# Kernel optimization log

Measured on AMD Instinct MI355X. Metric: run time of the kernel, lower is better.

The kernel has to match this reference:

```python
import jax, jax.numpy as jnp
import numpy as np

# ---- module hyperparameters ----
B, L, F = 128, 720, 128
SEG = 24            # segment_length
NSEG = L // SEG     # 30 input segments
WIN = 15            # window_size
NPRED = 96 // SEG   # 4 prediction segments
D = 128             # encode_dim
H = 512             # hidden_dim
DECAY = 0.9
C = 1.0             # curvature
EPS = 1e-6
MAXN = 1.0 - 1e-5   # max radius of Poincare ball (c=1)
SQC = 1.0           # sqrt(C)

# ---- Poincare-ball manifold ops ----
def _sqnorm(x):
    return jnp.sum(x * x, axis=-1, keepdims=True)

def _norm(x):
    return jnp.sqrt(jnp.maximum(_sqnorm(x), EPS * EPS))

def _project(x):
    n = _norm(x)
    return jnp.where(n > MAXN, x * (MAXN / n), x)

def _artanh(x):
    return jnp.arctanh(jnp.clip(x, -1.0 + 1e-7, 1.0 - 1e-7))

def mobius_add(x, y):
    xy = jnp.sum(x * y, axis=-1, keepdims=True)
    x2, y2 = _sqnorm(x), _sqnorm(y)
    num = (1.0 + 2.0 * C * xy + C * y2) * x + (1.0 - C * x2) * y
    den = 1.0 + 2.0 * C * xy + C * C * x2 * y2
    return num / jnp.maximum(den, EPS)

def expmap0(v):
    n = _norm(v)
    return _project(jnp.tanh(SQC * n) * v / (SQC * n))

def logmap0(y):
    n = _norm(y)
    return _artanh(SQC * n) * y / (SQC * n)

def expmap(x, v):
    lam = 2.0 / jnp.maximum(1.0 - C * _sqnorm(x), EPS)
    n = _norm(v)
    second = jnp.tanh(SQC * lam * n / 2.0) * v / (SQC * n)
    return _project(mobius_add(x, second))

def logmap(x, y):
    d = mobius_add(-x, y)
    n = _norm(d)
    lam = 2.0 / jnp.maximum(1.0 - C * _sqnorm(x), EPS)
    return (2.0 / (SQC * lam)) * _artanh(SQC * n) * d / n


def setup_inputs() -> dict:
    key = jax.random.key(0)
    ks = jax.random.split(key, 12)
    s = 0.05
    return {
        'trend':           0.5 * jax.random.normal(ks[0], (B, L, F), jnp.float32),
        'seasonal_coarse': 0.5 * jax.random.normal(ks[1], (B, L, F), jnp.float32),
        'seasonal_fine':   0.5 * jax.random.normal(ks[2], (B, L, F), jnp.float32),
        'residual':        0.5 * jax.random.normal(ks[3], (B, L, F), jnp.float32),
        'W_t': s * jax.random.normal(ks[4], (SEG, D), jnp.float32), 'b_t': jnp.zeros((D,), jnp.float32),
        'W_c': s * jax.random.normal(ks[5], (SEG, D), jnp.float32), 'b_c': jnp.zeros((D,), jnp.float32),
        'W_f': s * jax.random.normal(ks[6], (SEG, D), jnp.float32), 'b_f': jnp.zeros((D,), jnp.float32),
        'W_r': s * jax.random.normal(ks[7], (SEG, D), jnp.float32), 'b_r': jnp.zeros((D,), jnp.float32),
        'alpha': jnp.array([0.5], jnp.float32),
        'W1': s * jax.random.normal(ks[8], (D, H), jnp.float32), 'b1': jnp.zeros((H,), jnp.float32),
        'W2': s * jax.random.normal(ks[9], (H, SEG), jnp.float32), 'b2': jnp.zeros((SEG,), jnp.float32),
    }


def reference(trend, seasonal_coarse, seasonal_fine, residual,
              W_t, b_t, W_c, b_c, W_f, b_f, W_r, b_r,
              alpha, W1, b1, W2, b2):
    b, l, f = trend.shape

    def collapse(x):  # [B,L,F] -> [B*F, NSEG, SEG]
        return x.transpose(0, 2, 1).reshape(b * f, NSEG, SEG)

    t_s, c_s, f_s, r_s = map(collapse, (trend, seasonal_coarse, seasonal_fine, residual))

    # per-segment tangent encoding (channel-independent, shared params)
    tan = (jnp.einsum('bns,sd->bnd', t_s, W_t) + b_t
           + jnp.einsum('bns,sd->bnd', c_s, W_c) + b_c
           + jnp.einsum('bns,sd->bnd', f_s, W_f) + b_f
           + jnp.einsum('bns,sd->bnd', r_s, W_r) + b_r)
    z = expmap0(tan)                     # [BF, NSEG, D] on the ball
    z_cur = z[:, -WIN:, :]

    idx = jnp.arange(WIN - 1, dtype=jnp.float32)
    w = DECAY ** (WIN - 2 - idx)
    w = w / w.sum()

    preds, latents = [], []
    for _ in range(NPRED):
        z_last = z_cur[:, -1]
        vel = logmap(z_cur[:, :-1], z_cur[:, 1:])
        avg_v = jnp.sum(vel * w[None, :, None], axis=1)    # [BF, D]
        z_next = expmap(z_last, alpha * avg_v)             # dynamics step
        latents.append(z_next)
        # reconstruction head: logmap0 -> MLP -> segment
        t0 = logmap0(z_next)
        seg = jax.nn.relu(t0 @ W1 + b1) @ W2 + b2          # [BF, SEG]
        preds.append(seg)
        z_cur = jnp.concatenate([z_cur[:, 1:], z_next[:, None]], axis=1)

    p = jnp.stack(preds, axis=1).reshape(b * f, NPRED * SEG)
    predictions = p.reshape(b, f, NPRED * SEG).transpose(0, 2, 1)  # [B, pred_len, F]
    return predictions
```

## Files before the change

### kernel.cpp

```cpp
#include <hip/hip_runtime.h>
#include <hip/hip_bf16.h>

namespace {
constexpr int kL = 720, kF = 128;
constexpr int kWin = 15;
constexpr float kEps = 1e-6f;
constexpr float kMaxN = 1.0f - 1e-5f;
constexpr int kT0off = 360;
constexpr int XROW = 388;
constexpr int ZTR = 132;
constexpr size_t kOffT0   = 0;
constexpr size_t kOffW1   = 16777216;
constexpr size_t kOffW2   = kOffW1 + 131072;
constexpr size_t kOffWcat = kOffW2 + 32768;
constexpr size_t kOffBsum = kOffWcat + 49152;
constexpr size_t kOffHid  = 17825792;
constexpr size_t kWsSplit = kOffHid + 67108864;
}

typedef float f32x4 __attribute__((ext_vector_type(4)));
typedef short s16x8 __attribute__((ext_vector_type(8)));

__device__ __forceinline__ float rcp_f(float x) { return __builtin_amdgcn_rcpf(x); }
__device__ __forceinline__ float sqrt_f(float x) { return __builtin_amdgcn_sqrtf(x); }
__device__ __forceinline__ float tanh_f(float x) {
  float t = __builtin_amdgcn_exp2f(x * -2.8853900817779268f);
  return (1.0f - t) * rcp_f(1.0f + t);
}
__device__ __forceinline__ float artanh_f(float n) {
  float nc = fminf(n, 1.0f - 1e-7f);
  return 0.34657359027997264f * __builtin_amdgcn_logf((1.0f + nc) * rcp_f(1.0f - nc));
}

extern "C" __global__ __launch_bounds__(256)
void mwhf_prep(const float* __restrict__ W1, const float* __restrict__ W2,
               const float* __restrict__ W_t, const float* __restrict__ W_c,
               const float* __restrict__ W_f, const float* __restrict__ W_r,
               const float* __restrict__ b_t, const float* __restrict__ b_c,
               const float* __restrict__ b_f, const float* __restrict__ b_r,
               __hip_bfloat16* __restrict__ W1bf, __hip_bfloat16* __restrict__ W2bf,
               float* __restrict__ Wcat, float* __restrict__ bsum)
{
  const int b = blockIdx.x, tid = threadIdx.x;
  if (b < 64) {
    const int n0 = b * 8;
    for (int e = tid; e < 1024; e += 256) {
      int n_l = e & 7, k = e >> 3;
      W1bf[(size_t)(n0 + n_l) * 128 + k] = __float2bfloat16(W1[(size_t)k * 512 + n0 + n_l]);
    }
  } else if (b < 68) {
    const int k0 = (b - 64) * 128;
    for (int e = tid; e < 4096; e += 256) {
      int p = e >> 7, k_l = e & 127;
      float v = (p < 24) ? W2[(size_t)(k0 + k_l) * 24 + p] : 0.0f;
      W2bf[(size_t)p * 512 + k0 + k_l] = __float2bfloat16(v);
    }
  } else if (b < 72) {
    const int st = b - 68;
    const float* src = (st == 0) ? W_t : (st == 1) ? W_c : (st == 2) ? W_f : W_r;
    for (int e = tid; e < 3072; e += 256) Wcat[st * 3072 + e] = src[e];
  } else {
    if (tid < 128) bsum[tid] = b_t[tid] + b_c[tid] + b_f[tid] + b_r[tid];
  }
}

extern "C" __global__ __launch_bounds__(256, 4)
void mwhf_k1(const float* __restrict__ trend,
             const float* __restrict__ seas_c,
             const float* __restrict__ seas_f,
             const float* __restrict__ resid,
             const float* __restrict__ Wcat, const float* __restrict__ bsum,
             const float* __restrict__ alpha,
             __hip_bfloat16* __restrict__ t0_out)
{
  __shared__ float ublk[4 * kWin * ZTR];
  __shared__ float z2t[64];

  const int tid = threadIdx.x;
  const int bix = blockIdx.x;
  const int bb = (bix & 7) * 16 + (bix >> 8);
  const int f0 = ((bix >> 3) & 31) * 4;
  const int row0 = bb * 128 + f0;

  {
    float* xs = ublk;
    const float* ptrs[4] = {trend, seas_c, seas_f, resid};
    for (int e = tid; e < 1440; e += 256) {
      int seg = e / 96;
      int k = e - seg * 96;
      int st = k / 24, s = k - st * 24;
      const float* p = ptrs[st];
      float4 v = *(const float4*)&p[(size_t)(bb * kL + kT0off + seg * 24 + s) * kF + f0];
      *(float4*)&ublk[seg * XROW + k * 4] = v;
      (void)xs;
    }
  }
  __syncthreads();

  const int seg = tid >> 4;
  const int dg  = tid & 15;
  const bool act = (seg < kWin);
  float acc[4][8];
  float scale4[4], zz24[4];
  if (act) {
#pragma unroll
    for (int r = 0; r < 4; ++r)
#pragma unroll
      for (int j = 0; j < 8; ++j) acc[r][j] = 0.f;
    const float* xrow = &ublk[seg * XROW];
    const float* wp = Wcat + dg * 8;
#pragma unroll 4
    for (int k = 0; k < 96; ++k) {
      float4 x4 = *(const float4*)&xrow[k * 4];
      float4 wa = *(const float4*)&wp[k * 128];
      float4 wb = *(const float4*)&wp[k * 128 + 4];
      float w8[8] = {wa.x, wa.y, wa.z, wa.w, wb.x, wb.y, wb.z, wb.w};
#pragma unroll
      for (int j = 0; j < 8; ++j) {
        acc[0][j] += x4.x * w8[j];
        acc[1][j] += x4.y * w8[j];
        acc[2][j] += x4.z * w8[j];
        acc[3][j] += x4.w * w8[j];
      }
    }
    float b8[8];
    *(float4*)&b8[0] = *(const float4*)&bsum[dg * 8];
    *(float4*)&b8[4] = *(const float4*)&bsum[dg * 8 + 4];
    float part[4];
#pragma unroll
    for (int r = 0; r < 4; ++r) {
      part[r] = 0.f;
#pragma unroll
      for (int j = 0; j < 8; ++j) {
        acc[r][j] += b8[j];
        part[r] += acc[r][j] * acc[r][j];
      }
    }
#pragma unroll
    for (int m = 1; m <= 8; m <<= 1)
#pragma unroll
      for (int r = 0; r < 4; ++r) part[r] += __shfl_xor(part[r], m);
#pragma unroll
    for (int r = 0; r < 4; ++r) {
      float v2 = part[r];
      float nv = sqrt_f(fmaxf(v2, 1e-12f));
      float sc = tanh_f(nv) * rcp_f(nv);
      float y2 = sc * sc * v2;
      float yn = sqrt_f(fmaxf(y2, 1e-12f));
      float proj = (yn > kMaxN) ? (kMaxN * rcp_f(yn)) : 1.0f;
      scale4[r] = sc * proj;
      zz24[r] = y2 * proj * proj;
    }
  }
  __syncthreads();
  if (act) {
#pragma unroll
    for (int r = 0; r < 4; ++r) {
      float o8[8];
#pragma unroll
      for (int j = 0; j < 8; ++j) o8[j] = acc[r][j] * scale4[r];
      float* zp = &ublk[(r * kWin + seg) * ZTR + dg * 8];
      *(float4*)&zp[0] = *(const float4*)&o8[0];
      *(float4*)&zp[4] = *(const float4*)&o8[4];
      if (dg == 0) z2t[r * 16 + seg] = zz24[r];
    }
  }
  __syncthreads();

  {
    const int w = tid >> 6;
    const int l = tid & 63;
    float zx[19], zy[19], z2a[19], pd[18];
#pragma unroll
    for (int j = 0; j < 15; ++j) {
      float2 v = *(const float2*)&ublk[(w * kWin + j) * ZTR + 2 * l];
      zx[j] = v.x; zy[j] = v.y;
      z2a[j] = z2t[w * 16 + j];
    }
#pragma unroll
    for (int j = 0; j < 14; ++j) pd[j] = zx[j] * zx[j + 1] + zy[j] * zy[j + 1];
#pragma unroll
    for (int m = 1; m <= 32; m <<= 1)
#pragma unroll
      for (int j = 0; j < 14; ++j) pd[j] += __shfl_xor(pd[j], m);

    const float alp = alpha[0];
    float W14[14];
    {
      float wv = 1.f, ss = 0.f;
      W14[13] = 1.f;
#pragma unroll
      for (int i = 12; i >= 0; --i) { wv *= 0.9f; W14[i] = wv; }
#pragma unroll
      for (int i = 0; i < 14; ++i) ss += W14[i];
      float inv = 1.f / ss;
#pragma unroll
      for (int i = 0; i < 14; ++i) W14[i] *= inv;
    }

#pragma unroll
    for (int it = 0; it < 4; ++it) {
      float avx = 0.f, avy = 0.f;
#pragma unroll
      for (int i = 0; i < 14; ++i) {
        const int j = it + i, y = j + 1;
        float x2 = z2a[j], y2 = z2a[y], dp = pd[j];
        float A = 1.f - 2.f * dp + y2;
        float Bq = 1.f - x2;
        float den = fmaxf(1.f - 2.f * dp + x2 * y2, kEps);
        float invd = rcp_f(den);
        float d2 = (A * A * x2 - 2.f * A * Bq * dp + Bq * Bq * y2) * (invd * invd);
        float n = sqrt_f(fmaxf(d2, 1e-12f));
        float coef = fmaxf(Bq, kEps) * artanh_f(n) * rcp_f(n);
        float wi = W14[i] * coef * invd;
        avx += wi * (Bq * zx[y] - A * zx[j]);
        avy += wi * (Bq * zy[y] - A * zy[j]);
      }
      float vx = alp * avx, vy = alp * avy;
      const int pl = it + 14;
      float x2l = z2a[pl];
      float v2 = vx * vx + vy * vy;
      float xdv = zx[pl] * vx + zy[pl] * vy;
#pragma unroll
      for (int m = 1; m <= 32; m <<= 1) {
        v2 += __shfl_xor(v2, m);
        xdv += __shfl_xor(xdv, m);
      }
      float nv = sqrt_f(fmaxf(v2, 1e-12f));
      float lam = 2.f * rcp_f(fmaxf(1.f - x2l, kEps));
      float co = tanh_f(0.5f * lam * nv) * rcp_f(nv);
      float s2 = co * co * v2;
      float xy = co * xdv;
      float P = 1.f + 2.f * xy + s2;
      float Q = 1.f - x2l;
      float den2 = fmaxf(1.f + 2.f * xy + x2l * s2, kEps);
      float invd2 = rcp_f(den2);
      float znx = (P * zx[pl] + Q * co * vx) * invd2;
      float zny = (P * zy[pl] + Q * co * vy) * invd2;
      float zn2 = (P * P * x2l + 2.f * P * Q * xy + Q * Q * s2) * (invd2 * invd2);
      float pdn = (P * x2l + Q * xy) * invd2;
      float yn = sqrt_f(fmaxf(zn2, 1e-12f));
      float proj = (yn > kMaxN) ? (kMaxN * rcp_f(yn)) : 1.f;
      znx *= proj; zny *= proj;
      zn2 *= proj * proj;
      pdn *= proj;
      zx[15 + it] = znx; zy[15 + it] = zny;
      z2a[15 + it] = zn2;
      pd[14 + it] = pdn;
      float n0 = sqrt_f(fmaxf(zn2, 1e-12f));
      float fac = artanh_f(n0) * rcp_f(n0);
      __hip_bfloat162 hv;
      hv.x = __float2bfloat16(fac * znx);
      hv.y = __float2bfloat16(fac * zny);
      *(__hip_bfloat162*)(t0_out + ((size_t)(row0 + w) * 4 + it) * 128 + 2 * l) = hv;
    }
  }
}

extern "C" __global__ __launch_bounds__(256, 4)
void mwhf_k2a(const __hip_bfloat16* __restrict__ t0g,
              const __hip_bfloat16* __restrict__ W1bf,
              const float* __restrict__ b1,
              __hip_bfloat16* __restrict__ hid)
{
  const int tid = threadIdx.x;
  const int w = tid >> 6, lane = tid & 63;
  const int l16 = lane & 15, quad = lane >> 4;
  const int mbase = blockIdx.x * 32;
  const int ng = w * 128;

  s16x8 afr[2][4];
#pragma unroll
  for (int s = 0; s < 2; ++s)
#pragma unroll
    for (int kc = 0; kc < 4; ++kc)
      afr[s][kc] = *(const s16x8*)(t0g + (size_t)(mbase + s * 16 + l16) * 128 + kc * 32 + quad * 8);

  f32x4 acc[2][8];
#pragma unroll
  for (int s = 0; s < 2; ++s)
#pragma unroll
    for (int t = 0; t < 8; ++t) acc[s][t] = (f32x4)0.f;

#pragma unroll
  for (int t = 0; t < 8; ++t) {
    const __hip_bfloat16* bp = W1bf + (size_t)(ng + t * 16 + l16) * 128 + quad * 8;
#pragma unroll
    for (int kc = 0; kc < 4; ++kc) {
      s16x8 bfr = *(const s16x8*)(bp + kc * 32);
      acc[0][t] = __builtin_amdgcn_mfma_f32_16x16x32_bf16(afr[0][kc], bfr, acc[0][t], 0, 0, 0);
      acc[1][t] = __builtin_amdgcn_mfma_f32_16x16x32_bf16(afr[1][kc], bfr, acc[1][t], 0, 0, 0);
    }
  }
#pragma unroll
  for (int t = 0; t < 8; ++t) {
    const int n = ng + t * 16 + l16;
    float bv = b1[n];
#pragma unroll
    for (int s = 0; s < 2; ++s)
#pragma unroll
      for (int r = 0; r < 4; ++r) {
        int m = mbase + s * 16 + quad * 4 + r;
        float h = fmaxf(acc[s][t][r] + bv, 0.f);
        hid[(size_t)m * 512 + n] = __float2bfloat16(h);
      }
  }
}

extern "C" __global__ __launch_bounds__(256, 4)
void mwhf_k2b(const __hip_bfloat16* __restrict__ hid,
              const __hip_bfloat16* __restrict__ W2bf,
              const float* __restrict__ b2,
              float* __restrict__ outp)
{
  const int tid = threadIdx.x;
  const int w = tid >> 6, lane = tid & 63;
  const int l16 = lane & 15, quad = lane >> 4;
  const int mb = (blockIdx.x * 4 + w) * 32;

  f32x4 acc[2][2];
#pragma unroll
  for (int s = 0; s < 2; ++s)
#pragma unroll
    for (int t = 0; t < 2; ++t) acc[s][t] = (f32x4)0.f;

#pragma unroll 4
  for (int kc = 0; kc < 16; ++kc) {
    s16x8 a0 = *(const s16x8*)(hid + (size_t)(mb + l16) * 512 + kc * 32 + quad * 8);
    s16x8 a1 = *(const s16x8*)(hid + (size_t)(mb + 16 + l16) * 512 + kc * 32 + quad * 8);
#pragma unroll
    for (int t = 0; t < 2; ++t) {
      s16x8 bfr = *(const s16x8*)(W2bf + (size_t)(t * 16 + l16) * 512 + kc * 32 + quad * 8);
      acc[0][t] = __builtin_amdgcn_mfma_f32_16x16x32_bf16(a0, bfr, acc[0][t], 0, 0, 0);
      acc[1][t] = __builtin_amdgcn_mfma_f32_16x16x32_bf16(a1, bfr, acc[1][t], 0, 0, 0);
    }
  }
#pragma unroll
  for (int t = 0; t < 2; ++t) {
    const int p = t * 16 + l16;
    if (p < 24) {
      float bv = b2[p];
#pragma unroll
      for (int s = 0; s < 2; ++s)
#pragma unroll
        for (int r = 0; r < 4; ++r) {
          int m = mb + s * 16 + quad * 4 + r;
          int bbi = m >> 9, it = m & 3, f = (m >> 2) & 127;
          outp[(size_t)bbi * 12288 + (it * 24 + p) * 128 + f] = acc[s][t][r] + bv;
        }
    }
  }
}

extern "C" __global__ __launch_bounds__(256)
void mwhf_k2f(const __hip_bfloat16* __restrict__ t0g,
              const __hip_bfloat16* __restrict__ W1bf,
              const __hip_bfloat16* __restrict__ W2bf,
              const float* __restrict__ b1, const float* __restrict__ b2,
              float* __restrict__ outp)
{
  __shared__ __align__(16) char smem[147456];
  s16x8* Av   = (s16x8*)smem;
  s16x8* W1v  = (s16x8*)(smem + 16384);
  s16x8* W2v  = (s16x8*)(smem + 16384);
  float* red  = (float*)(smem + 49152);
  __hip_bfloat16* hid = (__hip_bfloat16*)(smem + 81920);
  s16x8* hidv = (s16x8*)(smem + 81920);

  const int tid = threadIdx.x;
  const int m0 = blockIdx.x * 64;
  const int w = tid >> 6, lane = tid & 63;
  const int l16 = lane & 15, quad = lane >> 4;

  {
    const s16x8* src = (const s16x8*)(t0g + (size_t)m0 * 128);
    for (int e = tid; e < 1024; e += 256) {
      int m = e >> 4, c = e & 15;
      Av[m * 16 + (c ^ (m & 7))] = src[e];
    }
  }
  f32x4 acc[4][4];
  for (int nh = 0; nh < 2; ++nh) {
    __syncthreads();
    {
      const s16x8* src = (const s16x8*)W1bf + (size_t)nh * 4096;
      for (int e = tid; e < 4096; e += 256) {
        int n = e >> 4, c = e & 15;
        W1v[n * 16 + (c ^ (n & 7))] = src[e];
      }
    }
    __syncthreads();
#pragma unroll
    for (int s = 0; s < 4; ++s)
#pragma unroll
      for (int t = 0; t < 4; ++t) acc[s][t] = (f32x4)0.f;
#pragma unroll
    for (int ks = 0; ks < 4; ++ks) {
      s16x8 a[4];
#pragma unroll
      for (int s = 0; s < 4; ++s)
        a[s] = Av[(s * 16 + l16) * 16 + ((ks * 4 + quad) ^ (l16 & 7))];
#pragma unroll
      for (int t = 0; t < 4; ++t) {
        int nl = w * 64 + t * 16 + l16;
        s16x8 bfr = W1v[nl * 16 + ((ks * 4 + quad) ^ (nl & 7))];
#pragma unroll
        for (int s = 0; s < 4; ++s)
          acc[s][t] = __builtin_amdgcn_mfma_f32_16x16x32_bf16(a[s], bfr, acc[s][t], 0, 0, 0);
      }
    }
#pragma unroll
    for (int t = 0; t < 4; ++t) {
      int nabs = nh * 256 + w * 64 + t * 16 + l16;
      float bv = b1[nabs];
#pragma unroll
      for (int s = 0; s < 4; ++s)
#pragma unroll
        for (int r = 0; r < 4; ++r) {
          int m = s * 16 + quad * 4 + r;
          float h = fmaxf(acc[s][t][r] + bv, 0.f);
          hid[m * 512 + (nabs ^ ((m & 7) << 3))] = __float2bfloat16(h);
        }
    }
  }
  __syncthreads();
  {
    const s16x8* src = (const s16x8*)W2bf;
    for (int e = tid; e < 2048; e += 256) {
      int p = e >> 6, c = e & 63;
      W2v[p * 64 + (c ^ (p & 7))] = src[e];
    }
  }
  __syncthreads();
  {
    f32x4 a2[2];
    a2[0] = (f32x4)0.f; a2[1] = (f32x4)0.f;
    const int m = w * 16 + l16;
#pragma unroll 4
    for (int ks = 0; ks < 16; ++ks) {
      s16x8 av = hidv[m * 64 + ((ks * 4 + quad) ^ (l16 & 7))];
#pragma unroll
      for (int t = 0; t < 2; ++t) {
        s16x8 bfr = W2v[(t * 16 + l16) * 64 + ((ks * 4 + quad) ^ (l16 & 7))];
        a2[t] = __builtin_amdgcn_mfma_f32_16x16x32_bf16(av, bfr, a2[t], 0, 0, 0);
      }
    }
#pragma unroll
    for (int t = 0; t < 2; ++t)
#pragma unroll
      for (int r = 0; r < 4; ++r) {
        int p = t * 16 + l16;
        if (p < 24) red[(w * 16 + quad * 4 + r) * 25 + p] = a2[t][r];
      }
  }
  __syncthreads();
  {
    const int bbi = m0 >> 9;
    const int f0 = (m0 >> 2) & 127;
    for (int e = tid; e < 1536; e += 256) {
      int fi = e & 15;
      int rest = e >> 4;
      int p = rest % 24;
      int it = rest / 24;
      outp[(size_t)bbi * 12288 + rest * 128 + f0 + fi] = red[(fi * 4 + it) * 25 + p] + b2[p];
    }
  }
}

extern "C" void kernel_launch(void* const* d_in, const int* in_sizes, int n_in,
                              void* d_out, int out_size, void* d_ws, size_t ws_size,
                              hipStream_t stream) {
  (void)in_sizes; (void)n_in; (void)out_size;
  const float* trend = (const float*)d_in[0];
  const float* sc    = (const float*)d_in[1];
  const float* sf    = (const float*)d_in[2];
  const float* rs    = (const float*)d_in[3];
  const float* W_t   = (const float*)d_in[4];
  const float* b_t   = (const float*)d_in[5];
  const float* W_c   = (const float*)d_in[6];
  const float* b_c   = (const float*)d_in[7];
  const float* W_f   = (const float*)d_in[8];
  const float* b_f   = (const float*)d_in[9];
  const float* W_r   = (const float*)d_in[10];
  const float* b_r   = (const float*)d_in[11];
  const float* alpha = (const float*)d_in[12];
  const float* W1    = (const float*)d_in[13];
  const float* b1    = (const float*)d_in[14];
  const float* W2    = (const float*)d_in[15];
  const float* b2    = (const float*)d_in[16];

  char* ws = (char*)d_ws;
  __hip_bfloat16* t0   = (__hip_bfloat16*)(ws + kOffT0);
  __hip_bfloat16* W1bf = (__hip_bfloat16*)(ws + kOffW1);
  __hip_bfloat16* W2bf = (__hip_bfloat16*)(ws + kOffW2);
  float* Wcat = (float*)(ws + kOffWcat);
  float* bsum = (float*)(ws + kOffBsum);
  __hip_bfloat16* hid = (__hip_bfloat16*)(ws + kOffHid);
  float* outp = (float*)d_out;

  hipLaunchKernelGGL(mwhf_prep, dim3(73), dim3(256), 0, stream,
                     W1, W2, W_t, W_c, W_f, W_r, b_t, b_c, b_f, b_r,
                     W1bf, W2bf, Wcat, bsum);
  hipLaunchKernelGGL(mwhf_k1, dim3(4096), dim3(256), 0, stream,
                     trend, sc, sf, rs, Wcat, bsum, alpha, t0);
  if (ws_size >= kWsSplit) {
    hipLaunchKernelGGL(mwhf_k2a, dim3(2048), dim3(256), 0, stream, t0, W1bf, b1, hid);
    hipLaunchKernelGGL(mwhf_k2b, dim3(512), dim3(256), 0, stream, hid, W2bf, b2, outp);
  } else {
    hipLaunchKernelGGL(mwhf_k2f, dim3(1024), dim3(256), 0, stream,
                       t0, W1bf, W2bf, b1, b2, outp);
  }
}
```

Before: 390.1 us.

## Compute segment encoder GEMM with split-bf16 MFMA instead of scalar FP32

Replaces the scalar FP32 FMA loop for the segment-encoding projection with bf16 MFMA instructions. Both inputs and weights are split into three bf16 pieces (hi/mid/lo) so that near-FP32 accuracy is kept using six MFMAs per tile. The weights are pre-split and transposed in the prep kernel, and the input tile is split on load into LDS. The occupancy hint is lowered from 4 to 3 blocks, and the extra split/convert work adds VALU and LDS traffic in exchange for the MFMA throughput.

```diff
diff --git a/kernel.cpp b/kernel.cpp
--- a/kernel.cpp
+++ b/kernel.cpp
@@ -7,13 +7,13 @@
 constexpr float kEps = 1e-6f;
 constexpr float kMaxN = 1.0f - 1e-5f;
 constexpr int kT0off = 360;
-constexpr int XROW = 388;
 constexpr int ZTR = 132;
+constexpr int AROW = 104;
 constexpr size_t kOffT0   = 0;
 constexpr size_t kOffW1   = 16777216;
 constexpr size_t kOffW2   = kOffW1 + 131072;
-constexpr size_t kOffWcat = kOffW2 + 32768;
-constexpr size_t kOffBsum = kOffWcat + 49152;
+constexpr size_t kOffBt   = kOffW2 + 32768;
+constexpr size_t kOffBsum = kOffBt + 73728;
 constexpr size_t kOffHid  = 17825792;
 constexpr size_t kWsSplit = kOffHid + 67108864;
 }
@@ -39,7 +39,8 @@
                const float* __restrict__ b_t, const float* __restrict__ b_c,
                const float* __restrict__ b_f, const float* __restrict__ b_r,
                __hip_bfloat16* __restrict__ W1bf, __hip_bfloat16* __restrict__ W2bf,
-               float* __restrict__ Wcat, float* __restrict__ bsum)
+               __hip_bfloat16* __restrict__ BtH, __hip_bfloat16* __restrict__ BtM,
+               __hip_bfloat16* __restrict__ BtL, float* __restrict__ bsum)
 {
   const int b = blockIdx.x, tid = threadIdx.x;
   if (b < 64) {
@@ -58,23 +59,42 @@
   } else if (b < 72) {
     const int st = b - 68;
     const float* src = (st == 0) ? W_t : (st == 1) ? W_c : (st == 2) ? W_f : W_r;
-    for (int e = tid; e < 3072; e += 256) Wcat[st * 3072 + e] = src[e];
+    for (int e = tid; e < 3072; e += 256) {
+      int s = e >> 7, d = e & 127;
+      float x = src[e];
+      __hip_bfloat16 h = __float2bfloat16(x);
+      float r1 = x - __bfloat162float(h);
+      __hip_bfloat16 m = __float2bfloat16(r1);
+      float r2 = r1 - __bfloat162float(m);
+      const int o = d * 96 + st * 24 + s;
+      BtH[o] = h;
+      BtM[o] = m;
+      BtL[o] = __float2bfloat16(r2);
+    }
   } else {
     if (tid < 128) bsum[tid] = b_t[tid] + b_c[tid] + b_f[tid] + b_r[tid];
   }
 }
 
-extern "C" __global__ __launch_bounds__(256, 4)
+extern "C" __global__ __launch_bounds__(256, 3)
 void mwhf_k1(const float* __restrict__ trend,
              const float* __restrict__ seas_c,
              const float* __restrict__ seas_f,
              const float* __restrict__ resid,
-             const float* __restrict__ Wcat, const float* __restrict__ bsum,
+             const __hip_bfloat16* __restrict__ BtH,
+             const __hip_bfloat16* __restrict__ BtM,
+             const __hip_bfloat16* __restrict__ BtL,
+             const float* __restrict__ bsum,
              const float* __restrict__ alpha,
              __hip_bfloat16* __restrict__ t0_out)
 {
-  __shared__ float ublk[4 * kWin * ZTR];
+  __shared__ __align__(16) char smem_raw[3 * 64 * AROW * 2];
   __shared__ float z2t[64];
+
+  float* ublk = (float*)smem_raw;
+  __hip_bfloat16* Ah = (__hip_bfloat16*)smem_raw;
+  __hip_bfloat16* Am = Ah + 64 * AROW;
+  __hip_bfloat16* Al = Am + 64 * AROW;
 
   const int tid = threadIdx.x;
   const int bix = blockIdx.x;
@@ -82,8 +102,14 @@
   const int f0 = ((bix >> 3) & 31) * 4;
   const int row0 = bb * 128 + f0;
 
-  {
-    float* xs = ublk;
+  for (int e = tid; e < 192; e += 256) {
+    int rr = e / 48, cc = e - rr * 48;
+    int off = (rr * 16 + 15) * AROW;
+    ((unsigned int*)(Ah + off))[cc] = 0u;
+    ((unsigned int*)(Am + off))[cc] = 0u;
+    ((unsigned int*)(Al + off))[cc] = 0u;
+  }
+  {
     const float* ptrs[4] = {trend, seas_c, seas_f, resid};
     for (int e = tid; e < 1440; e += 256) {
       int seg = e / 96;
@@ -91,49 +117,67 @@
       int st = k / 24, s = k - st * 24;
       const float* p = ptrs[st];
       float4 v = *(const float4*)&p[(size_t)(bb * kL + kT0off + seg * 24 + s) * kF + f0];
-      *(float4*)&ublk[seg * XROW + k * 4] = v;
-      (void)xs;
+      float xv[4] = {v.x, v.y, v.z, v.w};
+#pragma unroll
+      for (int f = 0; f < 4; ++f) {
+        int m = f * 16 + seg;
+        __hip_bfloat16 h = __float2bfloat16(xv[f]);
+        float r1 = xv[f] - __bfloat162float(h);
+        __hip_bfloat16 mm = __float2bfloat16(r1);
+        float r2 = r1 - __bfloat162float(mm);
+        Ah[m * AROW + k] = h;
+        Am[m * AROW + k] = mm;
+        Al[m * AROW + k] = __float2bfloat16(r2);
+      }
     }
   }
   __syncthreads();
 
-  const int seg = tid >> 4;
-  const int dg  = tid & 15;
-  const bool act = (seg < kWin);
-  float acc[4][8];
-  float scale4[4], zz24[4];
-  if (act) {
-#pragma unroll
-    for (int r = 0; r < 4; ++r)
-#pragma unroll
-      for (int j = 0; j < 8; ++j) acc[r][j] = 0.f;
-    const float* xrow = &ublk[seg * XROW];
-    const float* wp = Wcat + dg * 8;
-#pragma unroll 4
-    for (int k = 0; k < 96; ++k) {
-      float4 x4 = *(const float4*)&xrow[k * 4];
-      float4 wa = *(const float4*)&wp[k * 128];
-      float4 wb = *(const float4*)&wp[k * 128 + 4];
-      float w8[8] = {wa.x, wa.y, wa.z, wa.w, wb.x, wb.y, wb.z, wb.w};
-#pragma unroll
-      for (int j = 0; j < 8; ++j) {
-        acc[0][j] += x4.x * w8[j];
-        acc[1][j] += x4.y * w8[j];
-        acc[2][j] += x4.z * w8[j];
-        acc[3][j] += x4.w * w8[j];
-      }
-    }
-    float b8[8];
-    *(float4*)&b8[0] = *(const float4*)&bsum[dg * 8];
-    *(float4*)&b8[4] = *(const float4*)&bsum[dg * 8 + 4];
-    float part[4];
-#pragma unroll
-    for (int r = 0; r < 4; ++r) {
-      part[r] = 0.f;
-#pragma unroll
-      for (int j = 0; j < 8; ++j) {
-        acc[r][j] += b8[j];
-        part[r] += acc[r][j] * acc[r][j];
+  const int w = tid >> 6;
+  const int lane = tid & 63;
+  const int l16 = lane & 15, quad = lane >> 4;
+
+  f32x4 acc0[8];
+  float scale4[4], zz4[4];
+  {
+    f32x4 acc1[8];
+    s16x8 ah[3], am[3], al[3];
+    const int abase = (w * 16 + l16) * AROW + quad * 8;
+#pragma unroll
+    for (int ks = 0; ks < 3; ++ks) {
+      ah[ks] = *(const s16x8*)(Ah + abase + ks * 32);
+      am[ks] = *(const s16x8*)(Am + abase + ks * 32);
+      al[ks] = *(const s16x8*)(Al + abase + ks * 32);
+    }
+#pragma unroll
+    for (int t = 0; t < 8; ++t) { acc0[t] = (f32x4)0.f; acc1[t] = (f32x4)0.f; }
+    const __hip_bfloat16* bhp = BtH + l16 * 96 + quad * 8;
+    const __hip_bfloat16* bmp = BtM + l16 * 96 + quad * 8;
+    const __hip_bfloat16* blp = BtL + l16 * 96 + quad * 8;
+#pragma unroll
+    for (int t = 0; t < 8; ++t) {
+#pragma unroll
+      for (int ks = 0; ks < 3; ++ks) {
+        s16x8 bh = *(const s16x8*)(bhp + t * 1536 + ks * 32);
+        s16x8 bm = *(const s16x8*)(bmp + t * 1536 + ks * 32);
+        s16x8 bl = *(const s16x8*)(blp + t * 1536 + ks * 32);
+        acc0[t] = __builtin_amdgcn_mfma_f32_16x16x32_bf16(ah[ks], bh, acc0[t], 0, 0, 0);
+        acc1[t] = __builtin_amdgcn_mfma_f32_16x16x32_bf16(am[ks], bh, acc1[t], 0, 0, 0);
+        acc1[t] = __builtin_amdgcn_mfma_f32_16x16x32_bf16(ah[ks], bm, acc1[t], 0, 0, 0);
+        acc1[t] = __builtin_amdgcn_mfma_f32_16x16x32_bf16(al[ks], bh, acc1[t], 0, 0, 0);
+        acc1[t] = __builtin_amdgcn_mfma_f32_16x16x32_bf16(ah[ks], bl, acc1[t], 0, 0, 0);
+        acc1[t] = __builtin_amdgcn_mfma_f32_16x16x32_bf16(am[ks], bm, acc1[t], 0, 0, 0);
+      }
+    }
+    float part[4] = {0.f, 0.f, 0.f, 0.f};
+#pragma unroll
+    for (int t = 0; t < 8; ++t) {
+      float bv = bsum[t * 16 + l16];
+#pragma unroll
+      for (int r = 0; r < 4; ++r) {
+        float v = (acc0[t][r] + acc1[t][r]) + bv;
+        acc0[t][r] = v;
+        part[r] += v * v;
       }
     }
 #pragma unroll
@@ -149,26 +193,25 @@
       float yn = sqrt_f(fmaxf(y2, 1e-12f));
       float proj = (yn > kMaxN) ? (kMaxN * rcp_f(yn)) : 1.0f;
       scale4[r] = sc * proj;
-      zz24[r] = y2 * proj * proj;
+      zz4[r] = y2 * proj * proj;
     }
   }
   __syncthreads();
-  if (act) {
+  {
 #pragma unroll
     for (int r = 0; r < 4; ++r) {
-      float o8[8];
-#pragma unroll
-      for (int j = 0; j < 8; ++j) o8[j] = acc[r][j] * scale4[r];
-      float* zp = &ublk[(r * kWin + seg) * ZTR + dg * 8];
-      *(float4*)&zp[0] = *(const float4*)&o8[0];
-      *(float4*)&zp[4] = *(const float4*)&o8[4];
-      if (dg == 0) z2t[r * 16 + seg] = zz24[r];
+      int row = quad * 4 + r;
+      if (row < kWin) {
+#pragma unroll
+        for (int t = 0; t < 8; ++t)
+          ublk[(w * kWin + row) * ZTR + t * 16 + l16] = acc0[t][r] * scale4[r];
+        if (l16 == 0) z2t[w * 16 + row] = zz4[r];
+      }
     }
   }
   __syncthreads();
 
   {
-    const int w = tid >> 6;
     const int l = tid & 63;
     float zx[19], zy[19], z2a[19], pd[18];
 #pragma unroll
@@ -493,16 +536,18 @@
   __hip_bfloat16* t0   = (__hip_bfloat16*)(ws + kOffT0);
   __hip_bfloat16* W1bf = (__hip_bfloat16*)(ws + kOffW1);
   __hip_bfloat16* W2bf = (__hip_bfloat16*)(ws + kOffW2);
-  float* Wcat = (float*)(ws + kOffWcat);
+  __hip_bfloat16* BtH  = (__hip_bfloat16*)(ws + kOffBt);
+  __hip_bfloat16* BtM  = BtH + 12288;
+  __hip_bfloat16* BtL  = BtM + 12288;
   float* bsum = (float*)(ws + kOffBsum);
   __hip_bfloat16* hid = (__hip_bfloat16*)(ws + kOffHid);
   float* outp = (float*)d_out;
 
   hipLaunchKernelGGL(mwhf_prep, dim3(73), dim3(256), 0, stream,
                      W1, W2, W_t, W_c, W_f, W_r, b_t, b_c, b_f, b_r,
-                     W1bf, W2bf, Wcat, bsum);
+                     W1bf, W2bf, BtH, BtM, BtL, bsum);
   hipLaunchKernelGGL(mwhf_k1, dim3(4096), dim3(256), 0, stream,
-                     trend, sc, sf, rs, Wcat, bsum, alpha, t0);
+                     trend, sc, sf, rs, BtH, BtM, BtL, bsum, alpha, t0);
   if (ws_size >= kWsSplit) {
     hipLaunchKernelGGL(mwhf_k2a, dim3(2048), dim3(256), 0, stream, t0, W1bf, b1, hid);
     hipLaunchKernelGGL(mwhf_k2b, dim3(512), dim3(256), 0, stream, hid, W2bf, b2, outp);
```

After: 402.3 us. 3.1% more time.
